# Optimization experiments

Hardware: AMD Instinct MI355X
Metric: run time of the kernel (lower is better)

The kernel has to match this reference:

```python
import jax, jax.numpy as jnp
import numpy as np


def setup_inputs() -> dict:
    key = jax.random.key(0)
    k1, k2, k3 = jax.random.split(key, 3)
    B, T, D, U = 64, 1024, 256, 512
    inputs = jax.random.normal(k1, (B, T, D), dtype=jnp.float32)
    W_xh = jax.random.normal(k2, (D, U), dtype=jnp.float32) * (1.0 / np.sqrt(D))
    W_hh = jax.random.normal(k3, (U, U), dtype=jnp.float32) * (1.0 / np.sqrt(U))
    b_h = jnp.zeros((U,), dtype=jnp.float32)
    return {"inputs": inputs, "W_xh": W_xh, "W_hh": W_hh, "b_h": b_h}


def reference(inputs, W_xh, W_hh, b_h):
    # h_t = tanh(x_t @ W_xh + h_{t-1} @ W_hh + b_h); return_sequences=True
    B, T, D = inputs.shape
    U = W_hh.shape[0]
    # input projection is time-independent: precompute once (same math)
    xw = jnp.einsum('btd,du->btu', inputs, W_xh) + b_h  # (B, T, U)
    h0 = jnp.zeros((B, U), dtype=inputs.dtype)

    def step(h_prev, xw_t):
        h_t = jnp.tanh(xw_t + h_prev @ W_hh)
        return h_t, h_t

    _, hs = jax.lax.scan(step, h0, jnp.swapaxes(xw, 0, 1))  # (T, B, U)
    return jnp.swapaxes(hs, 0, 1)  # (B, T, U)
```

## Files before the change

### kernel.cpp

```cpp
#include <hip/hip_runtime.h>


typedef __attribute__((ext_vector_type(8))) short short8;
typedef __attribute__((ext_vector_type(4))) float f32x4;

#define T_SZ 1024
#define U_SZ 512

typedef union { unsigned long long q[2]; short8 v; } chunk16;

__device__ __forceinline__ unsigned short f2bf(float f){
  unsigned u = __float_as_uint(f);
  u += 0x7FFFu + ((u >> 16) & 1u);
  return (unsigned short)(u >> 16);
}
__device__ __forceinline__ float bf2f(unsigned short s){
  return __uint_as_float(((unsigned)s) << 16);
}

__global__ __launch_bounds__(256) void xw_gemm(const float* __restrict__ X,
                                               const float* __restrict__ W,
                                               const float* __restrict__ bias,
                                               float* __restrict__ out){
  __shared__ float As[16][132];
  __shared__ float Bs[16][68];
  const int tid = threadIdx.x;
  const int tx = tid & 15, ty = tid >> 4;
  const int row0 = blockIdx.x * 128;
  const int col0 = blockIdx.y * 64;
  float acc[8][4];
  #pragma unroll
  for(int a=0;a<8;a++)
    #pragma unroll
    for(int b=0;b<4;b++) acc[a][b]=0.f;

  for(int kc=0;kc<256;kc+=16){
    {
      const int m  = tid >> 2;
      const int kq = (tid & 3) * 4;
      #pragma unroll
      for(int h=0;h<2;h++){
        const float4 v = *(const float4*)&X[(size_t)(row0 + m + 64*h)*256 + kc + kq];
        As[kq+0][m+64*h]=v.x; As[kq+1][m+64*h]=v.y;
        As[kq+2][m+64*h]=v.z; As[kq+3][m+64*h]=v.w;
      }
    }
    {
      const int k = tid >> 4;
      const int c = (tid & 15) * 4;
      *(float4*)&Bs[k][c] = *(const float4*)&W[(size_t)(kc + k)*512 + col0 + c];
    }
    __syncthreads();
    #pragma unroll
    for(int k=0;k<16;k++){
      const float4 b4 = *(const float4*)&Bs[k][tx*4];
      const float4 a0 = *(const float4*)&As[k][ty*8];
      const float4 a1 = *(const float4*)&As[k][ty*8+4];
      const float av[8] = {a0.x,a0.y,a0.z,a0.w,a1.x,a1.y,a1.z,a1.w};
      const float bv[4] = {b4.x,b4.y,b4.z,b4.w};
      #pragma unroll
      for(int ii=0;ii<8;ii++)
        #pragma unroll
        for(int j=0;j<4;j++) acc[ii][j] = fmaf(av[ii], bv[j], acc[ii][j]);
    }
    __syncthreads();
  }
  #pragma unroll
  for(int ii=0;ii<8;ii++){
    const int row = row0 + ty*8 + ii;
    float4 o;
    o.x = acc[ii][0] + bias[col0+tx*4+0];
    o.y = acc[ii][1] + bias[col0+tx*4+1];
    o.z = acc[ii][2] + bias[col0+tx*4+2];
    o.w = acc[ii][3] + bias[col0+tx*4+3];
    *(float4*)&out[(size_t)row*512 + col0 + tx*4] = o;
  }
}

__global__ __launch_bounds__(256, 1) void rnn_rec(const float* __restrict__ Whh,
                                                  float* __restrict__ out,
                                                  int* __restrict__ flags,
                                                  unsigned short* __restrict__ ring){
  __shared__ unsigned short Ahi[16][520];
  __shared__ unsigned short Alo[16][520];
  __shared__ float red[2][64][4];

  const int bid = blockIdx.x;
  const int g  = bid & 3;
  const int i  = bid >> 2;
  const int tid = threadIdx.x;
  const int lane = tid & 63;
  const int w  = tid >> 6;
  const int nt = w & 1;
  const int kh = w >> 1;
  const int ln = lane & 15;
  const int lq = lane >> 4;
  const int b0 = g * 16;
  const int c0 = i * 32;
  const int ncol0 = c0 + nt * 16;

  short8 whi[8], wlo[8];
  #pragma unroll
  for(int kt=0;kt<8;kt++){
    short8 h8, l8;
    const int kb = kh*256 + kt*32 + lq*8;
    #pragma unroll
    for(int j=0;j<8;j++){
      const float wv = Whh[(size_t)(kb+j)*512 + ncol0 + ln];
      const unsigned short hb = f2bf(wv);
      const unsigned short lb = f2bf(wv - bf2f(hb));
      h8[j] = (short)hb; l8[j] = (short)lb;
    }
    whi[kt]=h8; wlo[kt]=l8;
  }
  for(int idx=tid; idx<16*520; idx+=256){
    ((unsigned short*)Ahi)[idx]=0;
    ((unsigned short*)Alo)[idx]=0;
  }
  __syncthreads();

  float xwv[4] = {0.f,0.f,0.f,0.f};
  float hprev[4] = {0.f,0.f,0.f,0.f};
  if(kh==0){
    #pragma unroll
    for(int r=0;r<4;r++)
      xwv[r] = out[((size_t)(b0 + lq*4 + r)*T_SZ + 0)*U_SZ + ncol0 + ln];
  }

  for(int t=0;t<T_SZ;t++){
    if(t>0){
      if(kh==0){
        #pragma unroll
        for(int r=0;r<4;r++)
          out[((size_t)(b0 + lq*4 + r)*T_SZ + (t-1))*U_SZ + ncol0 + ln] = hprev[r];
      }
      {
        const int s2 = lane >> 1;
        const int ntf = lane & 1;
        const int p = w + 4*s2;
        bool done = (lane>=8) || (p==i);
        while(__ballot(!done)){
          if(!done){
            const int f = __hip_atomic_load(&flags[((g*16+p)<<1)|ntf],
                                            __ATOMIC_RELAXED, __HIP_MEMORY_SCOPE_AGENT);
            done = (f >= t);
          }
        }
      }
      asm volatile("" ::: "memory");
      const size_t slot = (size_t)((t-1)&1);
      #pragma unroll
      for(int s3=0;s3<4;s3++){
        const int p = w + 4*s3;
        if(p==i) continue;
        const unsigned long long* rb =
            (const unsigned long long*)ring + ((slot*4 + g)*16 + p)*256;
        chunk16 ch, cl;
        ch.q[0] = __hip_atomic_load(rb + (size_t)lane*2 + 0,   __ATOMIC_RELAXED, __HIP_MEMORY_SCOPE_AGENT);
        ch.q[1] = __hip_atomic_load(rb + (size_t)lane*2 + 1,   __ATOMIC_RELAXED, __HIP_MEMORY_SCOPE_AGENT);
        cl.q[0] = __hip_atomic_load(rb + 128 + (size_t)lane*2, __ATOMIC_RELAXED, __HIP_MEMORY_SCOPE_AGENT);
        cl.q[1] = __hip_atomic_load(rb + 129 + (size_t)lane*2, __ATOMIC_RELAXED, __HIP_MEMORY_SCOPE_AGENT);
        const int kd = p*32 + lq*8;
        *(short8*)&Ahi[ln][kd] = ch.v;
        *(short8*)&Alo[ln][kd] = cl.v;
      }
    }
    __syncthreads();

    f32x4 c_hh = {0.f,0.f,0.f,0.f}, c_hl = {0.f,0.f,0.f,0.f}, c_lh = {0.f,0.f,0.f,0.f};
    #pragma unroll
    for(int kt=0;kt<8;kt++){
      const int k = kh*256 + kt*32 + lq*8;
      const short8 ah = *(const short8*)&Ahi[ln][k];
      const short8 al = *(const short8*)&Alo[ln][k];
      c_hh = __builtin_amdgcn_mfma_f32_16x16x32_bf16(ah, whi[kt], c_hh, 0, 0, 0);
      c_hl = __builtin_amdgcn_mfma_f32_16x16x32_bf16(ah, wlo[kt], c_hl, 0, 0, 0);
      c_lh = __builtin_amdgcn_mfma_f32_16x16x32_bf16(al, whi[kt], c_lh, 0, 0, 0);
    }
    f32x4 csum = c_hh + c_hl + c_lh;
    if(kh==1) *(f32x4*)&red[nt][lane][0] = csum;
    __syncthreads();
    if(kh==0){
      const f32x4 o = *(const f32x4*)&red[nt][lane][0];
      csum += o;
      #pragma unroll
      for(int r=0;r<4;r++){
        float pre = csum[r] + xwv[r];
        pre = fminf(fmaxf(pre, -12.f), 12.f);
        const float e = __expf(2.f*pre);
        const float h = (e-1.f)/(e+1.f);
        hprev[r] = h;
        const unsigned short hb = f2bf(h);
        const unsigned short lb = f2bf(h - bf2f(hb));
        Ahi[lq*4+r][ncol0+ln] = hb;
        Alo[lq*4+r][ncol0+ln] = lb;
      }
      {
        const int c  = lane & 31;
        const int m  = c >> 1;
        const int q  = nt*2 + (c & 1);
        const int sel = lane >> 5;
        const unsigned short* src = sel ? &Alo[m][c0 + q*8] : &Ahi[m][c0 + q*8];
        chunk16 ck; ck.v = *(const short8*)src;
        unsigned long long* rb = (unsigned long long*)ring
            + (((size_t)(t&1)*4 + g)*16 + i)*256 + (size_t)sel*128 + (size_t)(q*16 + m)*2;
        __hip_atomic_store(rb+0, ck.q[0], __ATOMIC_RELAXED, __HIP_MEMORY_SCOPE_AGENT);
        __hip_atomic_store(rb+1, ck.q[1], __ATOMIC_RELAXED, __HIP_MEMORY_SCOPE_AGENT);
      }
      asm volatile("s_waitcnt vmcnt(0)" ::: "memory");
      if(lane==0)
        __hip_atomic_store(&flags[((g*16+i)<<1)|nt], t+1,
                           __ATOMIC_RELAXED, __HIP_MEMORY_SCOPE_AGENT);
      {
        const int tn = (t < T_SZ-1) ? t+1 : t;
        #pragma unroll
        for(int r=0;r<4;r++)
          xwv[r] = out[((size_t)(b0 + lq*4 + r)*T_SZ + tn)*U_SZ + ncol0 + ln];
      }
    }
  }
  if(kh==0){
    #pragma unroll
    for(int r=0;r<4;r++)
      out[((size_t)(b0 + lq*4 + r)*T_SZ + (T_SZ-1))*U_SZ + ncol0 + ln] = hprev[r];
  }
}

extern "C" void kernel_launch(void* const* d_in, const int* in_sizes, int n_in,
                              void* d_out, int out_size, void* d_ws, size_t ws_size,
                              hipStream_t stream) {
  (void)in_sizes; (void)n_in; (void)out_size; (void)ws_size;
  const float* X   = (const float*)d_in[0];
  const float* Wxh = (const float*)d_in[1];
  const float* Whh = (const float*)d_in[2];
  const float* bh  = (const float*)d_in[3];
  float* out = (float*)d_out;

  int* flags = (int*)d_ws;
  unsigned short* ring = (unsigned short*)((char*)d_ws + 1024);

  xw_gemm<<<dim3(512, 8), 256, 0, stream>>>(X, Wxh, bh, out);
  rnn_rec<<<64, 256, 0, stream>>>(Whh, out, flags, ring);
}
```

Measured before the change: 3.688 ms.

## Replace flag-based handshake with tag bits embedded in ring data

Drops the separate per-block flag array and its polling loop. Each published word now carries a parity tag in the low bit of the lo-bf16 mantissa, and consumers spin directly on the data until all words show the expected tag. This removes the producer-side vmcnt wait plus flag store, and a round trip per step on the critical path of the recurrence. In exchange it sacrifices one bit of lo-part precision, and the block now also polls and copies its own slice. Barriers are replaced with explicit lgkmcnt-wait plus s_barrier.

```diff
diff --git a/kernel.cpp b/kernel.cpp
--- a/kernel.cpp
+++ b/kernel.cpp
@@ -3,11 +3,12 @@
 
 typedef __attribute__((ext_vector_type(8))) short short8;
 typedef __attribute__((ext_vector_type(4))) float f32x4;
+typedef __attribute__((ext_vector_type(4))) unsigned short ushort4v;
 
 #define T_SZ 1024
 #define U_SZ 512
 
-typedef union { unsigned long long q[2]; short8 v; } chunk16;
+#define BAR_LGKM() asm volatile("s_waitcnt lgkmcnt(0)\n\ts_barrier" ::: "memory")
 
 __device__ __forceinline__ unsigned short f2bf(float f){
   unsigned u = __float_as_uint(f);
@@ -79,8 +80,7 @@
 
 __global__ __launch_bounds__(256, 1) void rnn_rec(const float* __restrict__ Whh,
                                                   float* __restrict__ out,
-                                                  int* __restrict__ flags,
-                                                  unsigned short* __restrict__ ring){
+                                                  unsigned long long* __restrict__ ring){
   __shared__ unsigned short Ahi[16][520];
   __shared__ unsigned short Alo[16][520];
   __shared__ float red[2][64][4];
@@ -134,38 +134,50 @@
         for(int r=0;r<4;r++)
           out[((size_t)(b0 + lq*4 + r)*T_SZ + (t-1))*U_SZ + ncol0 + ln] = hprev[r];
       }
-      {
-        const int s2 = lane >> 1;
-        const int ntf = lane & 1;
-        const int p = w + 4*s2;
-        bool done = (lane>=8) || (p==i);
-        while(__ballot(!done)){
-          if(!done){
-            const int f = __hip_atomic_load(&flags[((g*16+p)<<1)|ntf],
-                                            __ATOMIC_RELAXED, __HIP_MEMORY_SCOPE_AGENT);
-            done = (f >= t);
-          }
+      const unsigned tagb = ((((unsigned)(t-1)) >> 1) & 1u) ^ 1u;
+      const unsigned long long* pb[4];
+      #pragma unroll
+      for(int s=0;s<4;s++){
+        const int p = 4*s + w;
+        pb[s] = ring + (((size_t)((t-1)&1)*4 + g)*16 + p)*256
+                     + (size_t)ln*16 + (size_t)lq*4;
+      }
+      unsigned long long v[4][4];
+      bool ok[4] = {false,false,false,false};
+      for(;;){
+        #pragma unroll
+        for(int s=0;s<4;s++) if(!ok[s]){
+          #pragma unroll
+          for(int u=0;u<4;u++)
+            v[s][u] = __hip_atomic_load(pb[s]+u, __ATOMIC_RELAXED,
+                                        __HIP_MEMORY_SCOPE_AGENT);
         }
-      }
-      asm volatile("" ::: "memory");
-      const size_t slot = (size_t)((t-1)&1);
-      #pragma unroll
-      for(int s3=0;s3<4;s3++){
-        const int p = w + 4*s3;
-        if(p==i) continue;
-        const unsigned long long* rb =
-            (const unsigned long long*)ring + ((slot*4 + g)*16 + p)*256;
-        chunk16 ch, cl;
-        ch.q[0] = __hip_atomic_load(rb + (size_t)lane*2 + 0,   __ATOMIC_RELAXED, __HIP_MEMORY_SCOPE_AGENT);
-        ch.q[1] = __hip_atomic_load(rb + (size_t)lane*2 + 1,   __ATOMIC_RELAXED, __HIP_MEMORY_SCOPE_AGENT);
-        cl.q[0] = __hip_atomic_load(rb + 128 + (size_t)lane*2, __ATOMIC_RELAXED, __HIP_MEMORY_SCOPE_AGENT);
-        cl.q[1] = __hip_atomic_load(rb + 129 + (size_t)lane*2, __ATOMIC_RELAXED, __HIP_MEMORY_SCOPE_AGENT);
-        const int kd = p*32 + lq*8;
-        *(short8*)&Ahi[ln][kd] = ch.v;
-        *(short8*)&Alo[ln][kd] = cl.v;
-      }
-    }
-    __syncthreads();
+        #pragma unroll
+        for(int s=0;s<4;s++) if(!ok[s]){
+          bool o = true;
+          #pragma unroll
+          for(int u=0;u<4;u++) o = o && ((((unsigned)v[s][u]) & 1u) == tagb);
+          ok[s] = o;
+        }
+        const bool all = ok[0] && ok[1] && ok[2] && ok[3];
+        if(__ballot(!all) == 0ull) break;
+      }
+      #pragma unroll
+      for(int s=0;s<4;s++){
+        const int p = 4*s + w;
+        short8 h8, l8;
+        #pragma unroll
+        for(int u=0;u<4;u++){
+          const unsigned w0 = (unsigned)v[s][u];
+          const unsigned w1 = (unsigned)(v[s][u] >> 32);
+          l8[2*u]   = (short)(w0 & 0xFFFFu); h8[2*u]   = (short)(w0 >> 16);
+          l8[2*u+1] = (short)(w1 & 0xFFFFu); h8[2*u+1] = (short)(w1 >> 16);
+        }
+        *(short8*)&Ahi[ln][p*32 + lq*8] = h8;
+        *(short8*)&Alo[ln][p*32 + lq*8] = l8;
+      }
+    }
+    BAR_LGKM();
 
     f32x4 c_hh = {0.f,0.f,0.f,0.f}, c_hl = {0.f,0.f,0.f,0.f}, c_lh = {0.f,0.f,0.f,0.f};
     #pragma unroll
@@ -179,10 +191,11 @@
     }
     f32x4 csum = c_hh + c_hl + c_lh;
     if(kh==1) *(f32x4*)&red[nt][lane][0] = csum;
-    __syncthreads();
+    BAR_LGKM();
     if(kh==0){
       const f32x4 o = *(const f32x4*)&red[nt][lane][0];
       csum += o;
+      const unsigned mytag = ((((unsigned)t) >> 1) & 1u) ^ 1u;
       #pragma unroll
       for(int r=0;r<4;r++){
         float pre = csum[r] + xwv[r];
@@ -191,26 +204,27 @@
         const float h = (e-1.f)/(e+1.f);
         hprev[r] = h;
         const unsigned short hb = f2bf(h);
-        const unsigned short lb = f2bf(h - bf2f(hb));
+        unsigned short lb = f2bf(h - bf2f(hb));
+        lb = (unsigned short)((lb & 0xFFFEu) | mytag);
         Ahi[lq*4+r][ncol0+ln] = hb;
         Alo[lq*4+r][ncol0+ln] = lb;
       }
       {
-        const int c  = lane & 31;
-        const int m  = c >> 1;
-        const int q  = nt*2 + (c & 1);
-        const int sel = lane >> 5;
-        const unsigned short* src = sel ? &Alo[m][c0 + q*8] : &Ahi[m][c0 + q*8];
-        chunk16 ck; ck.v = *(const short8*)src;
-        unsigned long long* rb = (unsigned long long*)ring
-            + (((size_t)(t&1)*4 + g)*16 + i)*256 + (size_t)sel*128 + (size_t)(q*16 + m)*2;
-        __hip_atomic_store(rb+0, ck.q[0], __ATOMIC_RELAXED, __HIP_MEMORY_SCOPE_AGENT);
-        __hip_atomic_store(rb+1, ck.q[1], __ATOMIC_RELAXED, __HIP_MEMORY_SCOPE_AGENT);
-      }
-      asm volatile("s_waitcnt vmcnt(0)" ::: "memory");
-      if(lane==0)
-        __hip_atomic_store(&flags[((g*16+i)<<1)|nt], t+1,
-                           __ATOMIC_RELAXED, __HIP_MEMORY_SCOPE_AGENT);
+        const int m  = lane >> 2;
+        const int q4 = lane & 3;
+        const ushort4v hi4 = *(const ushort4v*)&Ahi[m][c0 + nt*16 + q4*4];
+        const ushort4v lo4 = *(const ushort4v*)&Alo[m][c0 + nt*16 + q4*4];
+        const unsigned w0 = (unsigned)lo4.x | ((unsigned)hi4.x << 16);
+        const unsigned w1 = (unsigned)lo4.y | ((unsigned)hi4.y << 16);
+        const unsigned w2 = (unsigned)lo4.z | ((unsigned)hi4.z << 16);
+        const unsigned w3 = (unsigned)lo4.w | ((unsigned)hi4.w << 16);
+        const unsigned long long q0 = (unsigned long long)w0 | ((unsigned long long)w1 << 32);
+        const unsigned long long q1 = (unsigned long long)w2 | ((unsigned long long)w3 << 32);
+        unsigned long long* dst = ring + (((size_t)(t&1)*4 + g)*16 + i)*256
+                                       + (size_t)m*16 + (size_t)nt*8 + (size_t)q4*2;
+        __hip_atomic_store(dst+0, q0, __ATOMIC_RELAXED, __HIP_MEMORY_SCOPE_AGENT);
+        __hip_atomic_store(dst+1, q1, __ATOMIC_RELAXED, __HIP_MEMORY_SCOPE_AGENT);
+      }
       {
         const int tn = (t < T_SZ-1) ? t+1 : t;
         #pragma unroll
@@ -236,9 +250,8 @@
   const float* bh  = (const float*)d_in[3];
   float* out = (float*)d_out;
 
-  int* flags = (int*)d_ws;
-  unsigned short* ring = (unsigned short*)((char*)d_ws + 1024);
+  unsigned long long* ring = (unsigned long long*)d_ws;
 
   xw_gemm<<<dim3(512, 8), 256, 0, stream>>>(X, Wxh, bh, out);
-  rnn_rec<<<64, 256, 0, stream>>>(Whh, out, flags, ring);
-}
+  rnn_rec<<<64, 256, 0, stream>>>(Whh, out, ring);
+}
```

After: 5.015 ms. +36.0%, slower.
